# Kernel optimization log

Measured on AMD Instinct MI355X. Metric: run time of the kernel, lower is better.

Reference implementation:

```python
import jax, jax.numpy as jnp
import numpy as np

NEG_SLOPE = 0.2  # PyG GATConv default leaky_relu slope


def gat_layer(x, src, dst, W, a_src, a_dst, bias, heads, d, concat):
    # x: [N, in_dim]; src/dst: [E] (edges flow src -> dst, self-loops included)
    N = x.shape[0]
    h = (x @ W).reshape(N, heads, d)                      # [N, H, D]
    alpha_src = jnp.einsum('nhd,hd->nh', h, a_src)        # [N, H]
    alpha_dst = jnp.einsum('nhd,hd->nh', h, a_dst)        # [N, H]
    e = jax.nn.leaky_relu(alpha_src[src] + alpha_dst[dst], NEG_SLOPE)  # [E, H]
    # softmax over incoming edges of each destination node (segment softmax)
    m = jax.ops.segment_max(e, dst, num_segments=N)       # [N, H]
    ex = jnp.exp(e - m[dst])
    s = jax.ops.segment_sum(ex, dst, num_segments=N)      # [N, H]
    alpha = ex / s[dst]                                   # [E, H]
    msg = h[src] * alpha[..., None]                       # [E, H, D]
    out = jax.ops.segment_sum(msg, dst, num_segments=N)   # [N, H, D]
    out = out.reshape(N, heads * d) if concat else out.mean(axis=1)
    return out + bias


def setup_inputs() -> dict:
    key = jax.random.key(0)
    ks = jax.random.split(key, 12)
    N, E = 10000, 320000
    in_dim, hidden, heads, out_dim = 256, 64, 4, 40
    x = jax.random.normal(ks[0], (N, in_dim), dtype=jnp.float32)
    edge_index = jax.random.randint(ks[1], (2, E), 0, N, dtype=jnp.int64)
    s = 0.1
    return {
        'x': x,
        'edge_index': edge_index,
        'W1': jax.random.normal(ks[2], (in_dim, heads * hidden), jnp.float32) * s,
        'att_src1': jax.random.normal(ks[3], (heads, hidden), jnp.float32) * s,
        'att_dst1': jax.random.normal(ks[4], (heads, hidden), jnp.float32) * s,
        'bias1': jnp.zeros((heads * hidden,), jnp.float32),
        'W2': jax.random.normal(ks[5], (heads * hidden, out_dim), jnp.float32) * s,
        'att_src2': jax.random.normal(ks[6], (1, out_dim), jnp.float32) * s,
        'att_dst2': jax.random.normal(ks[7], (1, out_dim), jnp.float32) * s,
        'bias2': jnp.zeros((out_dim,), jnp.float32),
    }


def reference(x, edge_index, W1, att_src1, att_dst1, bias1, W2, att_src2, att_dst2, bias2):
    N = x.shape[0]
    # PyG GATConv adds self-loops by default
    loop = jnp.arange(N, dtype=edge_index.dtype)
    src = jnp.concatenate([edge_index[0], loop])
    dst = jnp.concatenate([edge_index[1], loop])
    h = gat_layer(x, src, dst, W1, att_src1, att_dst1, bias1, heads=4, d=64, concat=True)
    h = jax.nn.relu(h)
    out = gat_layer(h, src, dst, W2, att_src2, att_dst2, bias2, heads=1, d=40, concat=False)
    return jax.nn.log_softmax(out, axis=1)
```

## Files before the change

kernel.cpp:

```cpp
#include <hip/hip_runtime.h>
#include <hip/hip_bf16.h>
#include <math.h>

#define IN_DIM 256
#define C1 256
#define H1 4
#define OUT_DIM 40
#define W2PAD 48
#define NEG_SLOPE 0.2f
#define DSTRIDE 128

typedef __attribute__((ext_vector_type(8))) short bf16x8;
typedef __attribute__((ext_vector_type(4))) float f32x4;
typedef __attribute__((ext_vector_type(2))) float f32x2;

#define XS_LD 264

__device__ __forceinline__ unsigned short f2bf(float f) {
    union { float f; unsigned u; } c; c.f = f;
    unsigned r = c.u + 0x7fffu + ((c.u >> 16) & 1u);
    return (unsigned short)(r >> 16);
}

__device__ __forceinline__ unsigned char f2fp8(float f) {
    return (unsigned char)__builtin_amdgcn_cvt_pk_fp8_f32(f, 0.f, 0, false);
}

__device__ __forceinline__ float sel4(float4 v, int h) {
    float r = v.x;
    r = (h == 1) ? v.y : r;
    r = (h == 2) ? v.z : r;
    r = (h == 3) ? v.w : r;
    return r;
}

__device__ __forceinline__ float leaky(float v) {
    return (v >= 0.0f) ? v : NEG_SLOPE * v;
}

__global__ void k_prep(int* __restrict__ fill, const float* __restrict__ W1,
                       unsigned short* __restrict__ W1t, const float* __restrict__ W2,
                       unsigned short* __restrict__ W2t, const float* __restrict__ a_src2,
                       const float* __restrict__ a_dst2, float* __restrict__ w2s,
                       float* __restrict__ w2d, int N) {
    int t = threadIdx.x;
    int g = blockIdx.x * 256 + t;
    if (g < N) fill[g << 4] = 0;
    if (g < C1) {
        float s = 0.0f, d = 0.0f;
#pragma unroll
        for (int j = 0; j < OUT_DIM; ++j) {
            float w = W2[g * OUT_DIM + j];
            s += w * a_src2[j];
            d += w * a_dst2[j];
        }
        w2s[g] = s;
        w2d[g] = d;
    }
    if (g < W2PAD * C1) {
        int j = g >> 8, k = g & 255;
        W2t[g] = (j < OUT_DIM) ? f2bf(W2[k * OUT_DIM + j]) : 0;
    }
    __shared__ float s32[32][33];
    int b = blockIdx.x;
    int r0 = (b >> 3) * 32;
    int c0 = (b & 7) * 32;
    for (int i = t; i < 1024; i += 256) {
        int lr = i >> 5, lc = i & 31;
        s32[lr][lc] = W1[(r0 + lr) * 256 + c0 + lc];
    }
    __syncthreads();
    for (int i = t; i < 1024; i += 256) {
        int oc = i >> 5, ok = i & 31;
        W1t[(c0 + oc) * 256 + r0 + ok] = f2bf(s32[ok][oc]);
    }
}

__global__ void __launch_bounds__(256) k_fused1(
    const float* __restrict__ x, const unsigned short* __restrict__ W1t,
    const float* __restrict__ a_src, const float* __restrict__ a_dst,
    unsigned char* __restrict__ h1, float* __restrict__ as1, float* __restrict__ ad1,
    const int* __restrict__ ei, int* __restrict__ fill, unsigned short* __restrict__ srcs,
    int N, int E, int ET, int G1) {
    __shared__ unsigned short xs[64 * XS_LD];
    int t = threadIdx.x;

    if (blockIdx.x >= G1) {
        int eb = (blockIdx.x - G1) * 1024 + t;
#pragma unroll
        for (int k = 0; k < 4; ++k) {
            int e = eb + k * 256;
            if (e < ET) {
                int s, d;
                if (e < E) { s = ei[e]; d = ei[E + e]; }
                else       { s = e - E; d = s; }
                int pos = atomicAdd(&fill[d << 4], 1);
                srcs[(d << 7) + pos] = (unsigned short)s;
            }
        }
        return;
    }

    int n0 = blockIdx.x * 64;
    for (int i = t; i < 4096; i += 256) {
        int r = i >> 6, c4 = i & 63;
        int n = n0 + r;
        float4 v = (n < N) ? ((const float4*)x)[(size_t)n * 64 + c4]
                           : make_float4(0.f, 0.f, 0.f, 0.f);
        uint2 pk;
        pk.x = (unsigned)f2bf(v.x) | ((unsigned)f2bf(v.y) << 16);
        pk.y = (unsigned)f2bf(v.z) | ((unsigned)f2bf(v.w) << 16);
        *((uint2*)&xs[r * XS_LD + c4 * 4]) = pk;
    }
    __syncthreads();

    int wv = t >> 6, lane = t & 63;
    int quad = lane >> 4, ln = lane & 15;

    f32x4 acc[4][4];
#pragma unroll
    for (int mt = 0; mt < 4; ++mt)
#pragma unroll
        for (int nt = 0; nt < 4; ++nt) acc[mt][nt] = (f32x4){0.f, 0.f, 0.f, 0.f};

#pragma unroll
    for (int kb = 0; kb < 8; ++kb) {
        bf16x8 af[4], bf[4];
#pragma unroll
        for (int mt = 0; mt < 4; ++mt)
            af[mt] = *((bf16x8*)&xs[(mt * 16 + ln) * XS_LD + kb * 32 + quad * 8]);
#pragma unroll
        for (int nt = 0; nt < 4; ++nt)
            bf[nt] = *((const bf16x8*)(W1t + ((wv * 64 + nt * 16 + ln) * 256 + kb * 32 + quad * 8)));
#pragma unroll
        for (int mt = 0; mt < 4; ++mt)
#pragma unroll
            for (int nt = 0; nt < 4; ++nt)
                acc[mt][nt] = __builtin_amdgcn_mfma_f32_16x16x32_bf16(af[mt], bf[nt], acc[mt][nt], 0, 0, 0);
    }

    float asv[4], adv[4];
#pragma unroll
    for (int nt = 0; nt < 4; ++nt) {
        int col = wv * 64 + nt * 16 + ln;
        asv[nt] = a_src[col];
        adv[nt] = a_dst[col];
    }
#pragma unroll
    for (int mt = 0; mt < 4; ++mt) {
        float ds[4] = {0.f, 0.f, 0.f, 0.f};
        float dd[4] = {0.f, 0.f, 0.f, 0.f};
#pragma unroll
        for (int nt = 0; nt < 4; ++nt) {
#pragma unroll
            for (int r = 0; r < 4; ++r) {
                float v = acc[mt][nt][r];
                ds[r] += v * asv[nt];
                dd[r] += v * adv[nt];
            }
        }
#pragma unroll
        for (int r = 0; r < 4; ++r) {
            float vs = ds[r], vd = dd[r];
#pragma unroll
            for (int o = 1; o < 16; o <<= 1) {
                vs += __shfl_xor(vs, o);
                vd += __shfl_xor(vd, o);
            }
            if (ln == 0) {
                int node = n0 + mt * 16 + quad * 4 + r;
                if (node < N) {
                    as1[node * H1 + wv] = vs;
                    ad1[node * H1 + wv] = vd;
                }
            }
        }
    }

    __syncthreads();
    unsigned char* bt = (unsigned char*)xs;
#pragma unroll
    for (int mt = 0; mt < 4; ++mt)
#pragma unroll
        for (int nt = 0; nt < 4; ++nt)
#pragma unroll
            for (int r = 0; r < 4; ++r)
                bt[(mt * 16 + quad * 4 + r) * 256 + wv * 64 + nt * 16 + ln] = f2fp8(acc[mt][nt][r]);
    __syncthreads();
    const uint4* bt4 = (const uint4*)bt;
    uint4* h14 = (uint4*)(h1 + (size_t)n0 * C1);
    for (int i = t; i < 1024; i += 256) {
        int row = i >> 4;
        if (n0 + row < N) h14[i] = bt4[i];
    }
}

__global__ void __launch_bounds__(256) k_node1(
    const int* __restrict__ fill, const unsigned short* __restrict__ srcs,
    const float* __restrict__ as1f, const float* __restrict__ ad1f,
    const unsigned char* __restrict__ h1, const float* __restrict__ bias1,
    const float* __restrict__ w2s, const float* __restrict__ w2d,
    unsigned short* __restrict__ agg1b, float* __restrict__ as2,
    float* __restrict__ ad2, int N) {
    int w = threadIdx.x >> 6, lane = threadIdx.x & 63;
    int n = blockIdx.x * 4 + w;
    if (n >= N) return;
    __shared__ float4 es[4][64];
    int start = n << 7;
    int end = start + fill[n << 4];
    const float4* as4 = (const float4*)as1f;
    float4 adn = ((const float4*)ad1f)[n];
    int h = lane >> 4;
    const float* esw = (const float*)&es[w][0];

    float4 S4 = make_float4(0.f, 0.f, 0.f, 0.f);
    float ac0 = 0.f, ac1 = 0.f, ac2 = 0.f, ac3 = 0.f;

    for (int c = start; c < end; c += 64) {
        int cnt = min(64, end - c);
        int idx = c + lane;
        int sreg = (idx < end) ? (int)srcs[idx] : 0;
        float4 ex = make_float4(0.f, 0.f, 0.f, 0.f);
        if (idx < end) {
            float4 a = as4[sreg];
            ex.x = __expf(leaky(a.x + adn.x));
            ex.y = __expf(leaky(a.y + adn.y));
            ex.z = __expf(leaky(a.z + adn.z));
            ex.w = __expf(leaky(a.w + adn.w));
        }
        S4.x += ex.x; S4.y += ex.y; S4.z += ex.z; S4.w += ex.w;
        es[w][lane] = ex;

        int i = 0;
        for (; i + 7 < cnt; i += 8) {
            int s[8]; float a[8]; unsigned r[8];
#pragma unroll
            for (int k = 0; k < 8; ++k) {
                s[k] = __shfl(sreg, i + k);
                a[k] = esw[(i + k) * 4 + h];
            }
#pragma unroll
            for (int k = 0; k < 8; ++k)
                r[k] = ((const unsigned*)(h1 + (size_t)s[k] * C1))[lane];
#pragma unroll
            for (int k = 0; k < 8; ++k) {
                f32x2 lo = __builtin_amdgcn_cvt_pk_f32_fp8(r[k], false);
                f32x2 hi = __builtin_amdgcn_cvt_pk_f32_fp8(r[k], true);
                ac0 += a[k] * lo.x;
                ac1 += a[k] * lo.y;
                ac2 += a[k] * hi.x;
                ac3 += a[k] * hi.y;
            }
        }
        for (; i < cnt; ++i) {
            int s0 = __shfl(sreg, i);
            float a0 = esw[i * 4 + h];
            unsigned r0 = ((const unsigned*)(h1 + (size_t)s0 * C1))[lane];
            f32x2 lo = __builtin_amdgcn_cvt_pk_f32_fp8(r0, false);
            f32x2 hi = __builtin_amdgcn_cvt_pk_f32_fp8(r0, true);
            ac0 += a0 * lo.x;
            ac1 += a0 * lo.y;
            ac2 += a0 * hi.x;
            ac3 += a0 * hi.y;
        }
    }

#pragma unroll
    for (int o = 32; o > 0; o >>= 1) {
        S4.x += __shfl_xor(S4.x, o);
        S4.y += __shfl_xor(S4.y, o);
        S4.z += __shfl_xor(S4.z, o);
        S4.w += __shfl_xor(S4.w, o);
    }
    float iS = 1.0f / sel4(S4, h);
    float4 b = ((const float4*)bias1)[lane];
    float v0 = fmaxf(ac0 * iS + b.x, 0.f);
    float v1 = fmaxf(ac1 * iS + b.y, 0.f);
    float v2 = fmaxf(ac2 * iS + b.z, 0.f);
    float v3 = fmaxf(ac3 * iS + b.w, 0.f);
    uint2 pk;
    pk.x = (unsigned)f2bf(v0) | ((unsigned)f2bf(v1) << 16);
    pk.y = (unsigned)f2bf(v2) | ((unsigned)f2bf(v3) << 16);
    ((uint2*)(agg1b + (size_t)n * C1))[lane] = pk;

    float4 ws = ((const float4*)w2s)[lane];
    float4 wd = ((const float4*)w2d)[lane];
    float ps = v0 * ws.x + v1 * ws.y + v2 * ws.z + v3 * ws.w;
    float pd = v0 * wd.x + v1 * wd.y + v2 * wd.z + v3 * wd.w;
#pragma unroll
    for (int o = 32; o > 0; o >>= 1) {
        ps += __shfl_xor(ps, o);
        pd += __shfl_xor(pd, o);
    }
    if (lane == 0) { as2[n] = ps; ad2[n] = pd; }
}

__global__ void __launch_bounds__(256) k_gemm2m(
    const unsigned short* __restrict__ agg1b, const unsigned short* __restrict__ W2t,
    unsigned short* __restrict__ h2b, int N) {
    int t = threadIdx.x;
    int wv = t >> 6, lane = t & 63;
    int quad = lane >> 4, ln = lane & 15;
    int n0 = blockIdx.x * 64;
    int mrow = n0 + wv * 16 + ln;

    f32x4 acc[3];
#pragma unroll
    for (int nt = 0; nt < 3; ++nt) acc[nt] = (f32x4){0.f, 0.f, 0.f, 0.f};

#pragma unroll
    for (int kb = 0; kb < 8; ++kb) {
        bf16x8 af = *((const bf16x8*)(agg1b + (size_t)mrow * C1 + kb * 32 + quad * 8));
#pragma unroll
        for (int nt = 0; nt < 3; ++nt) {
            bf16x8 bfr = *((const bf16x8*)(W2t + ((nt * 16 + ln) * C1 + kb * 32 + quad * 8)));
            acc[nt] = __builtin_amdgcn_mfma_f32_16x16x32_bf16(af, bfr, acc[nt], 0, 0, 0);
        }
    }
#pragma unroll
    for (int nt = 0; nt < 3; ++nt) {
        int col = nt * 16 + ln;
        if (col < OUT_DIM) {
#pragma unroll
            for (int r = 0; r < 4; ++r) {
                int node = n0 + wv * 16 + quad * 4 + r;
                if (node < N) h2b[(size_t)node * OUT_DIM + col] = f2bf(acc[nt][r]);
            }
        }
    }
}

__global__ void __launch_bounds__(256) k_node2(
    const int* __restrict__ fill, const unsigned short* __restrict__ srcs,
    const float* __restrict__ as2, const float* __restrict__ ad2,
    const unsigned short* __restrict__ h2b, const float* __restrict__ bias2,
    float* __restrict__ out, int N) {
    int w = threadIdx.x >> 6, lane = threadIdx.x & 63;
    int n = blockIdx.x * 4 + w;
    if (n >= N) return;
    int start = n << 7;
    int end = start + fill[n << 4];
    float adn = ad2[n];
    float S = 0.f, acc0 = 0.f, acc1 = 0.f;
    bool act = lane < 20;

    for (int c = start; c < end; c += 64) {
        int cnt = min(64, end - c);
        int idx = c + lane;
        int sreg = (idx < end) ? (int)srcs[idx] : 0;
        float ex = (idx < end) ? __expf(leaky(as2[sreg] + adn)) : 0.f;
        S += ex;
        int i = 0;
        for (; i + 3 < cnt; i += 4) {
            int su[4]; float al[4]; unsigned rw[4];
#pragma unroll
            for (int k = 0; k < 4; ++k) {
                su[k] = __shfl(sreg, i + k);
                al[k] = __shfl(ex, i + k);
            }
#pragma unroll
            for (int k = 0; k < 4; ++k)
                rw[k] = act ? *(const unsigned*)(h2b + (size_t)su[k] * OUT_DIM + lane * 2) : 0u;
#pragma unroll
            for (int k = 0; k < 4; ++k) {
                acc0 += al[k] * __uint_as_float(rw[k] << 16);
                acc1 += al[k] * __uint_as_float(rw[k] & 0xffff0000u);
            }
        }
        for (; i < cnt; ++i) {
            int su0 = __shfl(sreg, i);
            float al0 = __shfl(ex, i);
            unsigned rw0 = act ? *(const unsigned*)(h2b + (size_t)su0 * OUT_DIM + lane * 2) : 0u;
            acc0 += al0 * __uint_as_float(rw0 << 16);
            acc1 += al0 * __uint_as_float(rw0 & 0xffff0000u);
        }
    }
#pragma unroll
    for (int o = 32; o > 0; o >>= 1) S += __shfl_xor(S, o);

    float v0 = act ? (acc0 / S + bias2[lane * 2]) : -INFINITY;
    float v1 = act ? (acc1 / S + bias2[lane * 2 + 1]) : -INFINITY;
    float mx = fmaxf(v0, v1);
#pragma unroll
    for (int o = 16; o > 0; o >>= 1) mx = fmaxf(mx, __shfl_xor(mx, o));
    float e0 = act ? __expf(v0 - mx) : 0.f;
    float e1 = act ? __expf(v1 - mx) : 0.f;
    float esum = e0 + e1;
#pragma unroll
    for (int o = 16; o > 0; o >>= 1) esum += __shfl_xor(esum, o);
    if (act) {
        float l = mx + logf(esum);
        out[(size_t)n * OUT_DIM + lane * 2]     = v0 - l;
        out[(size_t)n * OUT_DIM + lane * 2 + 1] = v1 - l;
    }
}

extern "C" void kernel_launch(void* const* d_in, const int* in_sizes, int n_in,
                              void* d_out, int out_size, void* d_ws, size_t ws_size,
                              hipStream_t stream) {
    const float* x        = (const float*)d_in[0];
    const int*   ei       = (const int*)d_in[1];
    const float* W1       = (const float*)d_in[2];
    const float* att_src1 = (const float*)d_in[3];
    const float* att_dst1 = (const float*)d_in[4];
    const float* bias1    = (const float*)d_in[5];
    const float* W2       = (const float*)d_in[6];
    const float* att_src2 = (const float*)d_in[7];
    const float* att_dst2 = (const float*)d_in[8];
    const float* bias2    = (const float*)d_in[9];
    float* out = (float*)d_out;

    const int N  = in_sizes[0] / IN_DIM;
    const int E  = in_sizes[1] / 2;
    const int ET = E + N;
    const int Npad = (N + 63) & ~63;

    char* base = (char*)d_ws;
    auto alloc = [&](size_t bytes) {
        char* p = base;
        base += (bytes + 255) & ~(size_t)255;
        return p;
    };
    unsigned char*  h1    = (unsigned char*)alloc((size_t)N * C1);
    unsigned short* W1t   = (unsigned short*)alloc((size_t)C1 * C1 * 2);
    unsigned short* W2t   = (unsigned short*)alloc((size_t)W2PAD * C1 * 2);
    unsigned short* agg1b = (unsigned short*)alloc((size_t)Npad * C1 * 2);
    unsigned short* h2b   = (unsigned short*)alloc((size_t)N * OUT_DIM * 2);
    float* as1   = (float*)alloc((size_t)N * H1 * 4);
    float* ad1   = (float*)alloc((size_t)N * H1 * 4);
    float* as2   = (float*)alloc((size_t)N * 4);
    float* ad2   = (float*)alloc((size_t)N * 4);
    float* w2s   = (float*)alloc((size_t)C1 * 4);
    float* w2d   = (float*)alloc((size_t)C1 * 4);
    int* fill    = (int*)alloc((size_t)N * 16 * 4);
    unsigned short* srcs = (unsigned short*)alloc((size_t)N * DSTRIDE * 2);

    const int G1 = (N + 63) / 64;
    const int GS = (ET + 1023) / 1024;

    k_prep<<<64, 256, 0, stream>>>(fill, W1, W1t, W2, W2t, att_src2, att_dst2, w2s, w2d, N);
    k_fused1<<<G1 + GS, 256, 0, stream>>>(x, W1t, att_src1, att_dst1, h1, as1, ad1,
                                          ei, fill, srcs, N, E, ET, G1);
    k_node1<<<(N + 3) / 4, 256, 0, stream>>>(fill, srcs, as1, ad1, h1, bias1, w2s, w2d,
                                             agg1b, as2, ad2, N);
    k_gemm2m<<<(N + 63) / 64, 256, 0, stream>>>(agg1b, W2t, h2b, N);
    k_node2<<<(N + 3) / 4, 256, 0, stream>>>(fill, srcs, as2, ad2, h2b, bias2, out, N);
}
```

Baseline: 142.6 us.

## Fuse layer-2 projection GEMM into the layer-1 aggregation kernel

Removes the separate k_gemm2m kernel and the agg1b global buffer. Each k_node1 block now writes its four aggregated bf16 rows into shared memory, synchronizes, and three of its waves run MFMA against W2t to emit h2b directly. This eliminates a kernel launch and a full global round-trip of the hidden activations. In exchange, 12 of the 16 MFMA rows are wasted, every block rereads W2t from cache, and a block barrier now ties the four node waves together, so imbalanced degrees can stall them.

```diff
diff --git a/kernel.cpp b/kernel.cpp
--- a/kernel.cpp
+++ b/kernel.cpp
@@ -200,16 +200,17 @@
     const float* __restrict__ as1f, const float* __restrict__ ad1f,
     const unsigned char* __restrict__ h1, const float* __restrict__ bias1,
     const float* __restrict__ w2s, const float* __restrict__ w2d,
-    unsigned short* __restrict__ agg1b, float* __restrict__ as2,
-    float* __restrict__ ad2, int N) {
+    const unsigned short* __restrict__ W2t, unsigned short* __restrict__ h2b,
+    float* __restrict__ as2, float* __restrict__ ad2, int N) {
     int w = threadIdx.x >> 6, lane = threadIdx.x & 63;
     int n = blockIdx.x * 4 + w;
-    if (n >= N) return;
+    bool valid = (n < N);
     __shared__ float4 es[4][64];
+    __shared__ unsigned short Abuf[16 * 256];
     int start = n << 7;
-    int end = start + fill[n << 4];
+    int end = start + (valid ? fill[n << 4] : 0);
     const float4* as4 = (const float4*)as1f;
-    float4 adn = ((const float4*)ad1f)[n];
+    float4 adn = valid ? ((const float4*)ad1f)[n] : make_float4(0.f, 0.f, 0.f, 0.f);
     int h = lane >> 4;
     const float* esw = (const float*)&es[w][0];
 
@@ -281,7 +282,7 @@
     uint2 pk;
     pk.x = (unsigned)f2bf(v0) | ((unsigned)f2bf(v1) << 16);
     pk.y = (unsigned)f2bf(v2) | ((unsigned)f2bf(v3) << 16);
-    ((uint2*)(agg1b + (size_t)n * C1))[lane] = pk;
+    ((uint2*)&Abuf[w * 256])[lane] = pk;
 
     float4 ws = ((const float4*)w2s)[lane];
     float4 wd = ((const float4*)w2d)[lane];
@@ -292,39 +293,25 @@
         ps += __shfl_xor(ps, o);
         pd += __shfl_xor(pd, o);
     }
-    if (lane == 0) { as2[n] = ps; ad2[n] = pd; }
-}
-
-__global__ void __launch_bounds__(256) k_gemm2m(
-    const unsigned short* __restrict__ agg1b, const unsigned short* __restrict__ W2t,
-    unsigned short* __restrict__ h2b, int N) {
-    int t = threadIdx.x;
-    int wv = t >> 6, lane = t & 63;
-    int quad = lane >> 4, ln = lane & 15;
-    int n0 = blockIdx.x * 64;
-    int mrow = n0 + wv * 16 + ln;
-
-    f32x4 acc[3];
-#pragma unroll
-    for (int nt = 0; nt < 3; ++nt) acc[nt] = (f32x4){0.f, 0.f, 0.f, 0.f};
-
-#pragma unroll
-    for (int kb = 0; kb < 8; ++kb) {
-        bf16x8 af = *((const bf16x8*)(agg1b + (size_t)mrow * C1 + kb * 32 + quad * 8));
-#pragma unroll
-        for (int nt = 0; nt < 3; ++nt) {
-            bf16x8 bfr = *((const bf16x8*)(W2t + ((nt * 16 + ln) * C1 + kb * 32 + quad * 8)));
-            acc[nt] = __builtin_amdgcn_mfma_f32_16x16x32_bf16(af, bfr, acc[nt], 0, 0, 0);
-        }
-    }
-#pragma unroll
-    for (int nt = 0; nt < 3; ++nt) {
-        int col = nt * 16 + ln;
-        if (col < OUT_DIM) {
+    if (lane == 0 && valid) { as2[n] = ps; ad2[n] = pd; }
+
+    __syncthreads();
+    if (w < 3) {
+        int quad = lane >> 4, ln = lane & 15;
+        f32x4 acc = (f32x4){0.f, 0.f, 0.f, 0.f};
+        const unsigned short* bbase = W2t + (w * 16 + ln) * 256;
+#pragma unroll
+        for (int kb = 0; kb < 8; ++kb) {
+            bf16x8 af = *((bf16x8*)&Abuf[ln * 256 + kb * 32 + quad * 8]);
+            bf16x8 bfr = *((const bf16x8*)(bbase + kb * 32 + quad * 8));
+            acc = __builtin_amdgcn_mfma_f32_16x16x32_bf16(af, bfr, acc, 0, 0, 0);
+        }
+        int col = w * 16 + ln;
+        if (col < OUT_DIM && quad == 0) {
 #pragma unroll
             for (int r = 0; r < 4; ++r) {
-                int node = n0 + wv * 16 + quad * 4 + r;
-                if (node < N) h2b[(size_t)node * OUT_DIM + col] = f2bf(acc[nt][r]);
+                int node = blockIdx.x * 4 + r;
+                if (node < N) h2b[(size_t)node * OUT_DIM + col] = f2bf(acc[r]);
             }
         }
     }
@@ -413,7 +400,6 @@
     const int N  = in_sizes[0] / IN_DIM;
     const int E  = in_sizes[1] / 2;
     const int ET = E + N;
-    const int Npad = (N + 63) & ~63;
 
     char* base = (char*)d_ws;
     auto alloc = [&](size_t bytes) {
@@ -424,7 +410,6 @@
     unsigned char*  h1    = (unsigned char*)alloc((size_t)N * C1);
     unsigned short* W1t   = (unsigned short*)alloc((size_t)C1 * C1 * 2);
     unsigned short* W2t   = (unsigned short*)alloc((size_t)W2PAD * C1 * 2);
-    unsigned short* agg1b = (unsigned short*)alloc((size_t)Npad * C1 * 2);
     unsigned short* h2b   = (unsigned short*)alloc((size_t)N * OUT_DIM * 2);
     float* as1   = (float*)alloc((size_t)N * H1 * 4);
     float* ad1   = (float*)alloc((size_t)N * H1 * 4);
@@ -442,7 +427,6 @@
     k_fused1<<<G1 + GS, 256, 0, stream>>>(x, W1t, att_src1, att_dst1, h1, as1, ad1,
                                           ei, fill, srcs, N, E, ET, G1);
     k_node1<<<(N + 3) / 4, 256, 0, stream>>>(fill, srcs, as1, ad1, h1, bias1, w2s, w2d,
-                                             agg1b, as2, ad2, N);
-    k_gemm2m<<<(N + 63) / 64, 256, 0, stream>>>(agg1b, W2t, h2b, N);
+                                             W2t, h2b, as2, ad2, N);
     k_node2<<<(N + 3) / 4, 256, 0, stream>>>(fill, srcs, as2, ad2, h2b, bias2, out, N);
 }
```

Measured after the change: 141.5 us (median of 2 runs). About the same (-0.8%).
